# Kernel tuning notes

Hardware: AMD Instinct MI355X
Metric: run time of the kernel (lower is better)

## Reference

```python
import jax, jax.numpy as jnp
import numpy as np

D_MODEL = 1024
N_HEADS = 16
HEAD_DIM = D_MODEL // N_HEADS
WINDOW = 512


def _rope(q, k, seq_len, head_dim):
    # interleaved RoPE, identical to the torch implementation
    theta = 1.0 / 10000.0 ** (jnp.arange(0, head_dim, 2, dtype=jnp.float32) / head_dim)
    pos = jnp.arange(seq_len, dtype=jnp.float32)
    freqs = jnp.outer(pos, theta)                      # [S, hD/2]
    cos_f = jnp.cos(freqs)[None, None]                 # [1,1,S,hD/2]
    sin_f = jnp.sin(freqs)[None, None]

    def rotate(x):
        x1, x2 = x[..., ::2], x[..., 1::2]
        return jnp.stack([x1 * cos_f - x2 * sin_f, x1 * sin_f + x2 * cos_f], axis=-1).reshape(x.shape)

    return rotate(q), rotate(k)


def _sliding_window_attn(q, k, v, W, scale):
    # chunked O(S*W) causal sliding-window attention
    B, nH, S, hD = q.shape
    n_chunks = (S + W - 1) // W
    pad_s = n_chunks * W - S
    k_pad = jnp.pad(k, ((0, 0), (0, 0), (W, pad_s), (0, 0)))
    v_pad = jnp.pad(v, ((0, 0), (0, 0), (W, pad_s), (0, 0)))
    q_pad = jnp.pad(q, ((0, 0), (0, 0), (0, pad_s), (0, 0)))
    q_c = q_pad.reshape(B, nH, n_chunks, W, hD)
    k_r = k_pad.reshape(B, nH, n_chunks + 1, W, hD)
    v_r = v_pad.reshape(B, nH, n_chunks + 1, W, hD)
    # window i = chunks [i, i+1] of the left-padded sequence (== torch unfold)
    k_c = jnp.concatenate([k_r[:, :, :-1], k_r[:, :, 1:]], axis=3)  # [B,nH,C,2W,hD]
    v_c = jnp.concatenate([v_r[:, :, :-1], v_r[:, :, 1:]], axis=3)
    attn = jnp.einsum('bhcqd,bhckd->bhcqk', q_c, k_c) * scale

    qi = jnp.arange(W)[:, None]
    ki = jnp.arange(2 * W)[None, :]
    cw_mask = (ki <= qi) | (ki > qi + W)               # [W, 2W]
    chunk_idx = jnp.arange(n_chunks)[:, None]
    abs_k = chunk_idx * W + ki - W                     # [C, 2W]
    pad_mask = (abs_k < 0) | (abs_k >= S)
    q_pos = jnp.arange(n_chunks * W).reshape(n_chunks, W)
    full_mask = cw_mask[None] | pad_mask[:, None, :] | (q_pos >= S)[..., None]  # [C,W,2W]

    attn = jnp.where(full_mask[None, None], -jnp.inf, attn)
    attn = jax.nn.softmax(attn, axis=-1)
    attn = jnp.nan_to_num(attn, nan=0.0)
    out = jnp.einsum('bhcqk,bhckd->bhcqd', attn, v_c)
    return out.reshape(B, nH, n_chunks * W, hD)[:, :, :S]


def _rmsnorm(x, w):
    eps = jnp.finfo(x.dtype).eps
    return x * jax.lax.rsqrt(jnp.mean(x * x, axis=-1, keepdims=True) + eps) * w


def _sdpa(q, k, v, scale):
    s = jnp.einsum('bhqd,bhkd->bhqk', q, k) * scale
    return jnp.einsum('bhqk,bhkd->bhqd', jax.nn.softmax(s, axis=-1), v)


def setup_inputs() -> dict:
    key = jax.random.key(0)
    ks = jax.random.split(key, 11)
    D = D_MODEL
    std = 0.02
    return {
        'x': jax.random.normal(ks[0], (2, 4096, D), jnp.float32),
        'landmarks': jax.random.normal(ks[1], (2, 256, D), jnp.float32),
        'archived_landmarks': jax.random.normal(ks[2], (2, 128, D), jnp.float32),
        'W_qkv': jax.random.normal(ks[3], (D, 3 * D), jnp.float32) * std,
        'W_lm': jax.random.normal(ks[4], (D, 2 * D), jnp.float32) * std,
        'W_arch': jax.random.normal(ks[5], (D, 2 * D), jnp.float32) * std,
        'W_o': jax.random.normal(ks[6], (D, D), jnp.float32) * std,
        'W_gate': jax.random.normal(ks[7], (3 * D, 2 * D), jnp.float32) * std,
        'g_local': jnp.ones((D,), jnp.float32),
        'g_lm': jnp.ones((D,), jnp.float32),
        'g_arch': jnp.ones((D,), jnp.float32),
    }


def reference(x, landmarks, archived_landmarks, W_qkv, W_lm, W_arch, W_o, W_gate, g_local, g_lm, g_arch):
    B, S, D = x.shape
    nH, hD = N_HEADS, HEAD_DIM
    scale = hD ** -0.5

    def rsh(t, L):
        return jnp.transpose(t.reshape(B, L, nH, hD), (0, 2, 1, 3))

    q, k, v = jnp.split(x @ W_qkv, 3, axis=-1)
    Q, K, V = rsh(q, S), rsh(k, S), rsh(v, S)
    Q, K = _rope(Q, K, S, hD)

    Weff = min(WINDOW, S)
    out_loc = _sliding_window_attn(Q, K, V, Weff, scale)  # S > Weff -> chunked path
    out_loc = _rmsnorm(jnp.transpose(out_loc, (0, 2, 1, 3)).reshape(B, S, D), g_local)

    L = landmarks.shape[1]
    K_lm, V_lm = jnp.split(landmarks @ W_lm, 2, axis=-1)
    out_lm = _sdpa(Q, rsh(K_lm, L), rsh(V_lm, L), scale)
    out_lm = _rmsnorm(jnp.transpose(out_lm, (0, 2, 1, 3)).reshape(B, S, D), g_lm)

    A = archived_landmarks.shape[1]
    K_a, V_a = jnp.split(archived_landmarks @ W_arch, 2, axis=-1)
    out_a = _sdpa(Q, rsh(K_a, A), rsh(V_a, A), scale)
    out_a = _rmsnorm(jnp.transpose(out_a, (0, 2, 1, 3)).reshape(B, S, D), g_arch)

    concat = jnp.concatenate([out_loc, out_lm, out_a], axis=-1)
    gate, value = jnp.split(concat @ W_gate, 2, axis=-1)
    return (jax.nn.silu(gate) * value) @ W_o
```

## Files before the change

### kernel.cpp

```cpp
#include <hip/hip_runtime.h>
#include <cstdint>
#include <cstddef>

typedef __bf16 bf16;
typedef __bf16 bf16x2 __attribute__((ext_vector_type(2)));
typedef __bf16 bf16x4 __attribute__((ext_vector_type(4)));
typedef __bf16 bf16x8 __attribute__((ext_vector_type(8)));
typedef float  f32x2 __attribute__((ext_vector_type(2)));
typedef float  f32x4 __attribute__((ext_vector_type(4)));

#define DEVFN __device__ __forceinline__
#define BAR()  asm volatile("s_barrier" ::: "memory")
#define VMW0() asm volatile("s_waitcnt vmcnt(0)" ::: "memory")
#define VMW3() asm volatile("s_waitcnt vmcnt(3)" ::: "memory")
#define VMW4() asm volatile("s_waitcnt vmcnt(4)" ::: "memory")
#define MFMA16 __builtin_amdgcn_mfma_f32_16x16x32_bf16

DEVFN void gld_lds16(void* lds, const void* g) {
  __builtin_amdgcn_global_load_lds(
      (__attribute__((address_space(1))) void*)g,
      (__attribute__((address_space(3))) void*)lds,
      16, 0, 0);
}

__global__ void cast_f32_bf16(const float* __restrict__ in, bf16* __restrict__ out, int n4) {
  int i = blockIdx.x * blockDim.x + threadIdx.x;
  if (i < n4) {
    f32x4 v = reinterpret_cast<const f32x4*>(in)[i];
    bf16x4 o;
    o[0] = (bf16)v[0]; o[1] = (bf16)v[1]; o[2] = (bf16)v[2]; o[3] = (bf16)v[3];
    reinterpret_cast<bf16x4*>(out)[i] = o;
  }
}

__global__ void transpose_cast(const float* __restrict__ in, bf16* __restrict__ out,
                               int R, int C) {
  __shared__ float t[32][33];
  int tx = threadIdx.x, ty = threadIdx.y;
  int c = blockIdx.x * 32 + tx;
  #pragma unroll
  for (int j = 0; j < 4; ++j) {
    int r = blockIdx.y * 32 + ty + j * 8;
    t[ty + j * 8][tx] = in[(size_t)r * C + c];
  }
  __syncthreads();
  int rr = blockIdx.y * 32 + tx;
  #pragma unroll
  for (int j = 0; j < 4; ++j) {
    int cc = blockIdx.x * 32 + ty + j * 8;
    out[(size_t)cc * R + rr] = (bf16)t[tx][ty + j * 8];
  }
}

__global__ void rope_table(float* __restrict__ tab) {
  int idx = blockIdx.x * 256 + threadIdx.x;
  int s = idx >> 5, i = idx & 31;
  float theta = powf(10000.f, -(float)(2 * i) * (1.f / 64.f));
  float f = (float)s * theta;
  tab[idx * 2]     = cosf(f);
  tab[idx * 2 + 1] = sinf(f);
}

__global__ __launch_bounds__(512) void gemm_gate4(
    const bf16* __restrict__ A, const bf16* __restrict__ Bt,
    bf16* __restrict__ G, int K) {
  __shared__ alignas(16) bf16 lds[2][2][2][256 * 32];
  const int tid = threadIdx.x;
  const int w = tid >> 6, l = tid & 63;
  const int l15 = l & 15, lg = l >> 4;
  const int wm = w >> 2, wn = w & 3;
  const int nwg = gridDim.x, qx = nwg >> 3;
  const int swz = (blockIdx.x & 7) * qx + (blockIdx.x >> 3);
  const int m0 = (swz >> 3) << 8;
  const int n0 = (swz & 7) << 7;
  const int nt = K >> 6;

  auto stage = [&](int b, int ab, int kk, int t) {
    const int k0 = (t << 6) + (kk << 5);
    #pragma unroll
    for (int i = 0; i < 2; ++i) {
      int u = i * 512 + tid;
      int row = u >> 2, slot = u & 3;
      int ss = slot ^ ((row >> 1) & 3);
      int grow;
      if (ab) {
        int q = row >> 6, o = row & 63;
        grow = (o < 32) ? (n0 + q * 32 + o) : (1024 + n0 + q * 32 + o - 32);
      } else {
        grow = m0 + row;
      }
      const bf16* src = ab ? Bt : A;
      gld_lds16(&lds[b][ab][kk][(i * 512 + w * 64) * 8],
                src + (size_t)grow * K + k0 + ss * 8);
    }
  };
  auto rd = [&](int b, int ab, int kk, int r) -> bf16x8 {
    return *reinterpret_cast<const bf16x8*>(
        &lds[b][ab][kk][(r << 5) + ((lg ^ ((r >> 1) & 3)) << 3)]);
  };

  f32x4 acc[8][4] = {};
  bf16x8 aLo[4], aHi[4], bfr[4];

  stage(0, 0, 0, 0);
  stage(0, 1, 0, 0);
  stage(0, 0, 1, 0);
  stage(0, 1, 1, 0);
  VMW4();
  BAR();

  for (int t = 0; t < nt; ++t) {
    const int c = t & 1;
    const bool st = (t + 1) < nt;
    #pragma unroll
    for (int f = 0; f < 4; ++f) aLo[f] = rd(c, 0, 0, wm * 128 + f * 16 + l15);
    #pragma unroll
    for (int f = 0; f < 4; ++f) bfr[f] = rd(c, 1, 0, wn * 64 + f * 16 + l15);
    if (st) stage(c ^ 1, 0, 0, t + 1);
    BAR();
    __builtin_amdgcn_s_setprio(1);
    #pragma unroll
    for (int mi = 0; mi < 4; ++mi)
      #pragma unroll
      for (int ni = 0; ni < 4; ++ni)
        acc[mi][ni] = MFMA16(aLo[mi], bfr[ni], acc[mi][ni], 0, 0, 0);
    __builtin_amdgcn_s_setprio(0);
    #pragma unroll
    for (int f = 0; f < 4; ++f) aHi[f] = rd(c, 0, 0, wm * 128 + (f + 4) * 16 + l15);
    BAR();
    if (st) stage(c ^ 1, 1, 0, t + 1);
    BAR();
    __builtin_amdgcn_s_setprio(1);
    #pragma unroll
    for (int mi = 0; mi < 4; ++mi)
      #pragma unroll
      for (int ni = 0; ni < 4; ++ni)
        acc[mi + 4][ni] = MFMA16(aHi[mi], bfr[ni], acc[mi + 4][ni], 0, 0, 0);
    __builtin_amdgcn_s_setprio(0);
    if (st) { VMW4(); } else { VMW0(); }
    BAR();
    #pragma unroll
    for (int f = 0; f < 4; ++f) aLo[f] = rd(c, 0, 1, wm * 128 + f * 16 + l15);
    #pragma unroll
    for (int f = 0; f < 4; ++f) bfr[f] = rd(c, 1, 1, wn * 64 + f * 16 + l15);
    if (st) stage(c ^ 1, 0, 1, t + 1);
    BAR();
    __builtin_amdgcn_s_setprio(1);
    #pragma unroll
    for (int mi = 0; mi < 4; ++mi)
      #pragma unroll
      for (int ni = 0; ni < 4; ++ni)
        acc[mi][ni] = MFMA16(aLo[mi], bfr[ni], acc[mi][ni], 0, 0, 0);
    __builtin_amdgcn_s_setprio(0);
    #pragma unroll
    for (int f = 0; f < 4; ++f) aHi[f] = rd(c, 0, 1, wm * 128 + (f + 4) * 16 + l15);
    BAR();
    if (st) stage(c ^ 1, 1, 1, t + 1);
    BAR();
    __builtin_amdgcn_s_setprio(1);
    #pragma unroll
    for (int mi = 0; mi < 4; ++mi)
      #pragma unroll
      for (int ni = 0; ni < 4; ++ni)
        acc[mi + 4][ni] = MFMA16(aHi[mi], bfr[ni], acc[mi + 4][ni], 0, 0, 0);
    __builtin_amdgcn_s_setprio(0);
    VMW4();
    BAR();
  }

  #pragma unroll
  for (int mi = 0; mi < 8; ++mi) {
    #pragma unroll
    for (int r = 0; r < 4; ++r) {
      int row = m0 + wm * 128 + mi * 16 + lg * 4 + r;
      bf16* grow = G + (size_t)row * 1024 + n0 + wn * 32 + l15;
      #pragma unroll
      for (int ni = 0; ni < 2; ++ni) {
        float g = acc[mi][ni][r], v = acc[mi][ni + 2][r];
        grow[ni * 16] = (bf16)((g / (1.f + __expf(-g))) * v);
      }
    }
  }
}

template<typename OT>
__global__ __launch_bounds__(512) void gemm256n128(
    const bf16* __restrict__ A, const bf16* __restrict__ Bt, OT* __restrict__ C,
    int M, int N, int K) {
  __shared__ alignas(16) bf16 ldsA[2][2][256 * 32];
  __shared__ alignas(16) bf16 ldsB[2][2][128 * 32];
  const int tid = threadIdx.x;
  const int w = tid >> 6, l = tid & 63;
  const int l15 = l & 15, lg = l >> 4;
  const int wm = w >> 1, wn = w & 1;
  const int nwg = gridDim.x, qx = nwg >> 3;
  const int swz = (blockIdx.x & 7) * qx + (blockIdx.x >> 3);
  const int gx = N >> 7;
  const int m0 = (swz / gx) << 8;
  const int n0 = (swz % gx) << 7;
  const int nt = K >> 6;

  auto stageA = [&](int b, int kk, int t) {
    const int k0 = (t << 6) + (kk << 5);
    #pragma unroll
    for (int i = 0; i < 2; ++i) {
      int u = i * 512 + tid;
      int row = u >> 2, slot = u & 3;
      int ss = slot ^ ((row >> 1) & 3);
      gld_lds16(&ldsA[b][kk][(i * 512 + w * 64) * 8],
                A + (size_t)(m0 + row) * K + k0 + ss * 8);
    }
  };
  auto stageB = [&](int b, int kk, int t) {
    const int k0 = (t << 6) + (kk << 5);
    int row = tid >> 2, slot = tid & 3;
    int ss = slot ^ ((row >> 1) & 3);
    gld_lds16(&ldsB[b][kk][(w * 64) * 8],
              Bt + (size_t)(n0 + row) * K + k0 + ss * 8);
  };
  auto rdA = [&](int b, int kk, int r) -> bf16x8 {
    return *reinterpret_cast<const bf16x8*>(
        &ldsA[b][kk][(r << 5) + ((lg ^ ((r >> 1) & 3)) << 3)]);
  };
  auto rdB = [&](int b, int kk, int r) -> bf16x8 {
    return *reinterpret_cast<const bf16x8*>(
        &ldsB[b][kk][(r << 5) + ((lg ^ ((r >> 1) & 3)) << 3)]);
  };

  f32x4 acc[4][4] = {};
  bf16x8 af[4], bf[4];

  stageA(0, 0, 0); stageB(0, 0, 0);
  stageA(0, 1, 0); stageB(0, 1, 0);
  VMW3();
  BAR();

  for (int t = 0; t < nt; ++t) {
    const int c = t & 1;
    const bool st = (t + 1) < nt;
    #pragma unroll
    for (int kk = 0; kk < 2; ++kk) {
      #pragma unroll
      for (int f = 0; f < 4; ++f) af[f] = rdA(c, kk, wm * 64 + f * 16 + l15);
      #pragma unroll
      for (int f = 0; f < 4; ++f) bf[f] = rdB(c, kk, wn * 64 + f * 16 + l15);
      if (st) { stageA(c ^ 1, kk, t + 1); stageB(c ^ 1, kk, t + 1); }
      BAR();
      __builtin_amdgcn_s_setprio(1);
      #pragma unroll
      for (int mi = 0; mi < 4; ++mi)
        #pragma unroll
        for (int ni = 0; ni < 4; ++ni)
          acc[mi][ni] = MFMA16(af[mi], bf[ni], acc[mi][ni], 0, 0, 0);
      __builtin_amdgcn_s_setprio(0);
      if (st) { VMW3(); }
      else if (kk == 0) { VMW0(); }
      BAR();
    }
  }

  #pragma unroll
  for (int mi = 0; mi < 4; ++mi) {
    #pragma unroll
    for (int r = 0; r < 4; ++r) {
      int row = m0 + wm * 64 + mi * 16 + lg * 4 + r;
      OT* crow = C + (size_t)row * N + n0 + wn * 64 + l15;
      #pragma unroll
      for (int ni = 0; ni < 4; ++ni) crow[ni * 16] = (OT)acc[mi][ni][r];
    }
  }
}

__global__ __launch_bounds__(256) void gemm_skt(
    const bf16* __restrict__ A, const bf16* __restrict__ Bt, float* __restrict__ C,
    int M, int N, int Ktot, int Kc) {
  __shared__ alignas(16) bf16 As[128 * 64];
  __shared__ alignas(16) bf16 Bs[128 * 64];
  int tid = threadIdx.x;
  int w = tid >> 6, l = tid & 63;
  int l15 = l & 15, lg = l >> 4;
  int m0 = blockIdx.y * 128;
  int n0 = blockIdx.x * 128;
  int sk = blockIdx.z;
  int kb = sk * Kc;
  float* Cs = C + (size_t)sk * M * N;
  int wr = (w >> 1) * 64, wc = (w & 1) * 64;
  f32x4 acc[4][4] = {};
  int nk = Kc >> 6;
  for (int kt = 0; kt < nk; ++kt) {
    int k0 = kb + (kt << 6);
    #pragma unroll
    for (int it = 0; it < 4; ++it) {
      int c = it * 256 + tid;
      int row = c >> 3, c8 = c & 7;
      gld_lds16(&As[(size_t)(it * 256 + w * 64) * 8],
                A + (size_t)(m0 + row) * Ktot + k0 + c8 * 8);
      gld_lds16(&Bs[(size_t)(it * 256 + w * 64) * 8],
                Bt + (size_t)(n0 + row) * Ktot + k0 + c8 * 8);
    }
    __syncthreads();
    #pragma unroll
    for (int kk = 0; kk < 64; kk += 32) {
      bf16x8 a[4], b[4];
      #pragma unroll
      for (int i = 0; i < 4; ++i)
        a[i] = *reinterpret_cast<const bf16x8*>(&As[(wr + i * 16 + l15) * 64 + kk + lg * 8]);
      #pragma unroll
      for (int i = 0; i < 4; ++i)
        b[i] = *reinterpret_cast<const bf16x8*>(&Bs[(wc + i * 16 + l15) * 64 + kk + lg * 8]);
      #pragma unroll
      for (int mi = 0; mi < 4; ++mi)
        #pragma unroll
        for (int ni = 0; ni < 4; ++ni)
          acc[mi][ni] = MFMA16(a[mi], b[ni], acc[mi][ni], 0, 0, 0);
    }
    __syncthreads();
  }
  #pragma unroll
  for (int mi = 0; mi < 4; ++mi) {
    #pragma unroll
    for (int r = 0; r < 4; ++r) {
      int row = m0 + wr + mi * 16 + lg * 4 + r;
      float* crow = Cs + (size_t)row * N + n0 + wc + l15;
      #pragma unroll
      for (int ni = 0; ni < 4; ++ni) crow[ni * 16] = acc[mi][ni][r];
    }
  }
}

__global__ void rope_qk(const bf16* __restrict__ qkv, const float* __restrict__ tab,
                        bf16* __restrict__ Qb, bf16* __restrict__ Kb) {
  int idx = blockIdx.x * 256 + threadIdx.x;
  int i = idx & 31;
  int h = (idx >> 5) & 15;
  int bs = idx >> 9;
  int s = bs & 4095;
  int b = bs >> 12;
  const bf16* row = qkv + (size_t)bs * 3072;
  bf16x2 q2 = *reinterpret_cast<const bf16x2*>(row + h * 64 + 2 * i);
  bf16x2 k2 = *reinterpret_cast<const bf16x2*>(row + 1024 + h * 64 + 2 * i);
  f32x2 cs = *reinterpret_cast<const f32x2*>(tab + s * 64 + 2 * i);
  float c = cs[0], sn = cs[1];
  float q0 = (float)q2[0], q1 = (float)q2[1];
  float k0 = (float)k2[0], k1 = (float)k2[1];
  size_t ob = (((size_t)(b * 16 + h) * 4096) + s) * 64 + 2 * i;
  bf16x2 qo, ko;
  qo[0] = (bf16)((q0 * c - q1 * sn) * 0.125f);
  qo[1] = (bf16)((q0 * sn + q1 * c) * 0.125f);
  ko[0] = (bf16)(k0 * c - k1 * sn);
  ko[1] = (bf16)(k0 * sn + k1 * c);
  *reinterpret_cast<bf16x2*>(Qb + ob) = qo;
  *reinterpret_cast<bf16x2*>(Kb + ob) = ko;
}

__global__ void kv_post(const bf16* __restrict__ kv, bf16* __restrict__ Kdst,
                        bf16* __restrict__ Vt, int Lk, int rs, int koff, int voff) {
  __shared__ float t[64][65];
  int s0 = blockIdx.x * 64;
  int h = blockIdx.y, b = blockIdx.z;
  int tid = threadIdx.x;
  int lane_d = tid & 63;
  int rq = tid >> 6;
  const bf16* base = kv + (size_t)b * Lk * rs;
  if (Kdst) {
    #pragma unroll
    for (int r = 0; r < 16; ++r) {
      int si = r * 4 + rq;
      Kdst[(((size_t)(b * 16 + h) * Lk) + s0 + si) * 64 + lane_d] =
          base[(size_t)(s0 + si) * rs + koff + h * 64 + lane_d];
    }
  }
  #pragma unroll
  for (int r = 0; r < 16; ++r) {
    int si = r * 4 + rq;
    t[si][lane_d] = (float)base[(size_t)(s0 + si) * rs + voff + h * 64 + lane_d];
  }
  __syncthreads();
  #pragma unroll
  for (int r = 0; r < 16; ++r) {
    int d = r * 4 + rq;
    Vt[(((size_t)(b * 16 + h) * 64) + d) * Lk + s0 + lane_d] = (bf16)t[lane_d][d];
  }
}

__global__ void kv_post4(const float* __restrict__ kv, bf16* __restrict__ Kdst,
                         bf16* __restrict__ Vt, int Lk, int Mtot) {
  __shared__ float t[64][65];
  int s0 = blockIdx.x * 64;
  int h = blockIdx.y, b = blockIdx.z;
  int tid = threadIdx.x;
  int lane_d = tid & 63;
  int rq = tid >> 6;
  const size_t slab = (size_t)Mtot * 2048;
  const float* base = kv + (size_t)b * Lk * 2048;
  #pragma unroll
  for (int r = 0; r < 16; ++r) {
    int si = r * 4 + rq;
    size_t o = (size_t)(s0 + si) * 2048 + h * 64 + lane_d;
    float kvv = base[o] + base[slab + o] + base[2 * slab + o] + base[3 * slab + o];
    size_t ov = o + 1024;
    float vvv = base[ov] + base[slab + ov] + base[2 * slab + ov] + base[3 * slab + ov];
    Kdst[(((size_t)(b * 16 + h) * Lk) + s0 + si) * 64 + lane_d] = (bf16)kvv;
    t[si][lane_d] = vvv;
  }
  __syncthreads();
  #pragma unroll
  for (int r = 0; r < 16; ++r) {
    int d = r * 4 + rq;
    Vt[(((size_t)(b * 16 + h) * 64) + d) * Lk + s0 + lane_d] = (bf16)t[lane_d][d];
  }
}

__global__ __launch_bounds__(256) void attn64(
    const bf16* __restrict__ Qb, const bf16* __restrict__ Kb,
    const bf16* __restrict__ Vt, bf16* __restrict__ outc) {
  constexpr int S = 4096;
  __shared__ alignas(16) bf16 Ks[2][64 * 64];
  __shared__ alignas(16) bf16 Vs[2][64 * 64];
  __shared__ alignas(16) bf16 Ps[4][16 * 72];
  int tid = threadIdx.x;
  int w = tid >> 6, l = tid & 63;
  int l15 = l & 15, lg = l >> 4;
  int qt = blockIdx.x, h = blockIdx.y, b = blockIdx.z;

  size_t qrow = (((size_t)(b * 16 + h) * S) + qt * 64 + w * 16 + l15) * 64;
  bf16x8 qf[2];
  qf[0] = *reinterpret_cast<const bf16x8*>(Qb + qrow + lg * 8);
  qf[1] = *reinterpret_cast<const bf16x8*>(Qb + qrow + 32 + lg * 8);
  const bf16* Kbase = Kb + ((size_t)(b * 16 + h) * S) * 64;
  const bf16* Vbase = Vt + ((size_t)(b * 16 + h) * 64) * S;

  float mrow = -1e30f, lsum = 0.f;
  f32x4 acc[4] = {};

  const int kt_hi = qt;
  const int kt_lo = qt >= 8 ? qt - 8 : 0;

  auto stage = [&](int buf, int kt) {
    const bf16* kg = Kbase + (size_t)kt * 64 * 64;
    #pragma unroll
    for (int it = 0; it < 2; ++it) {
      int u = it * 256 + tid;
      int row = u >> 3, sl = u & 7;
      gld_lds16(&Ks[buf][(it * 256 + w * 64) * 8], kg + row * 64 + (sl ^ (row & 7)) * 8);
    }
    #pragma unroll
    for (int it = 0; it < 2; ++it) {
      int u = it * 256 + tid;
      int row = u >> 3, sl = u & 7;
      gld_lds16(&Vs[buf][(it * 256 + w * 64) * 8],
                Vbase + (size_t)row * S + kt * 64 + (sl ^ (row & 7)) * 8);
    }
  };

  stage(0, kt_hi);

  int i = 0;
  for (int kt = kt_hi; kt >= kt_lo; --kt, ++i) {
    const int buf = i & 1;
    if (kt > kt_lo) { stage(buf ^ 1, kt - 1); VMW4(); } else { VMW0(); }
    BAR();

    f32x4 st[4] = {};
    #pragma unroll
    for (int kk = 0; kk < 2; ++kk) {
      #pragma unroll
      for (int f = 0; f < 4; ++f) {
        bf16x8 kf = *reinterpret_cast<const bf16x8*>(
            &Ks[buf][(f * 16 + l15) * 64 + (((kk * 4 + lg) ^ (l15 & 7)) << 3)]);
        st[f] = MFMA16(kf, qf[kk], st[f], 0, 0, 0);
      }
    }

    int qi = w * 16 + l15;
    if (kt == qt) {
      #pragma unroll
      for (int f = 0; f < 4; ++f)
        #pragma unroll
        for (int r = 0; r < 4; ++r)
          if (f * 16 + lg * 4 + r > qi) st[f][r] = -1e30f;
    } else if (kt == qt - 8) {
      #pragma unroll
      for (int f = 0; f < 4; ++f)
        #pragma unroll
        for (int r = 0; r < 4; ++r)
          if (f * 16 + lg * 4 + r <= qi) st[f][r] = -1e30f;
    }

    float rm = -1e30f;
    #pragma unroll
    for (int f = 0; f < 4; ++f)
      #pragma unroll
      for (int r = 0; r < 4; ++r) rm = fmaxf(rm, st[f][r]);
    rm = fmaxf(rm, __shfl_xor(rm, 16));
    rm = fmaxf(rm, __shfl_xor(rm, 32));
    float mnew = fmaxf(mrow, rm);
    float fsc = __expf(mrow - mnew);
    float ps = 0.f;
    #pragma unroll
    for (int f = 0; f < 4; ++f) {
      bf16x4 pv;
      #pragma unroll
      for (int r = 0; r < 4; ++r) {
        float p = __expf(st[f][r] - mnew);
        ps += p;
        pv[r] = (bf16)p;
      }
      *reinterpret_cast<bf16x4*>(&Ps[w][l15 * 72 + f * 16 + lg * 4]) = pv;
    }
    ps += __shfl_xor(ps, 16);
    ps += __shfl_xor(ps, 32);
    lsum = lsum * fsc + ps;
    mrow = mnew;

    #pragma unroll
    for (int r = 0; r < 4; ++r) {
      float fr = __shfl(fsc, lg * 4 + r);
      #pragma unroll
      for (int f = 0; f < 4; ++f) acc[f][r] *= fr;
    }

    #pragma unroll
    for (int kk = 0; kk < 2; ++kk) {
      bf16x8 pa = *reinterpret_cast<const bf16x8*>(&Ps[w][l15 * 72 + kk * 32 + lg * 8]);
      #pragma unroll
      for (int f = 0; f < 4; ++f) {
        bf16x8 vf = *reinterpret_cast<const bf16x8*>(
            &Vs[buf][(f * 16 + l15) * 64 + (((kk * 4 + lg) ^ (l15 & 7)) << 3)]);
        acc[f] = MFMA16(pa, vf, acc[f], 0, 0, 0);
      }
    }
    BAR();
  }

  float inv = 1.f / lsum;
  #pragma unroll
  for (int r = 0; r < 4; ++r) {
    float ir = __shfl(inv, lg * 4 + r);
    int srow = qt * 64 + w * 16 + lg * 4 + r;
    bf16* orow = outc + ((size_t)b * S + srow) * 3072 + h * 64 + l15;
    #pragma unroll
    for (int f = 0; f < 4; ++f) orow[f * 16] = (bf16)(acc[f][r] * ir);
  }
}

template<int LKV, int NQI>
__global__ __launch_bounds__(512) void attn_res(
    const bf16* __restrict__ Qb, const bf16* __restrict__ Kb,
    const bf16* __restrict__ Vt, bf16* __restrict__ outc, int col_off) {
  constexpr int S = 4096;
  __shared__ alignas(16) bf16 Ks[LKV * 64];
  __shared__ alignas(16) bf16 Vs[64 * LKV];
  __shared__ alignas(16) bf16 Ps[8][2][16 * 72];
  const int tid = threadIdx.x;
  const int w = tid >> 6, l = tid & 63;
  const int l15 = l & 15, lg = l >> 4;
  const int h = blockIdx.y, b = blockIdx.z;
  const bf16* Kg = Kb + ((size_t)(b * 16 + h) * LKV) * 64;
  const bf16* Vg = Vt + ((size_t)(b * 16 + h) * 64) * LKV;

  constexpr int NU = LKV / 64;
  constexpr int SPR = LKV / 8;
  #pragma unroll
  for (int i = 0; i < NU; ++i) {
    int u = i * 512 + tid;
    int row = u >> 3, sl = u & 7;
    gld_lds16(&Ks[(i * 512 + w * 64) * 8], Kg + row * 64 + (sl ^ (row & 7)) * 8);
  }
  #pragma unroll
  for (int i = 0; i < NU; ++i) {
    int u = i * 512 + tid;
    int row = u / SPR, sl = u % SPR;
    gld_lds16(&Vs[(i * 512 + w * 64) * 8],
              Vg + (size_t)row * LKV + ((sl & ~7) + ((sl & 7) ^ (row & 7))) * 8);
  }
  __syncthreads();

  for (int qi = 0; qi < NQI; ++qi) {
    const int Q0 = (blockIdx.x * NQI + qi) * 256 + w * 32;
    bf16x8 qf[2][2];
    #pragma unroll
    for (int c = 0; c < 2; ++c) {
      size_t qrow = (((size_t)(b * 16 + h) * S) + Q0 + c * 16 + l15) * 64;
      qf[c][0] = *reinterpret_cast<const bf16x8*>(Qb + qrow + lg * 8);
      qf[c][1] = *reinterpret_cast<const bf16x8*>(Qb + qrow + 32 + lg * 8);
    }
    float mrow[2] = {-30000.f, -30000.f}, lsum[2] = {0.f, 0.f};
    f32x4 acc[2][4] = {};

    #pragma unroll
    for (int kt = 0; kt < LKV / 64; ++kt) {
      f32x4 st[2][4] = {};
      #pragma unroll
      for (int kk = 0; kk < 2; ++kk) {
        #pragma unroll
        for (int f = 0; f < 4; ++f) {
          bf16x8 kf = *reinterpret_cast<const bf16x8*>(
              &Ks[(kt * 64 + f * 16 + l15) * 64 + (((kk * 4 + lg) ^ (l15 & 7)) << 3)]);
          #pragma unroll
          for (int c = 0; c < 2; ++c)
            st[c][f] = MFMA16(kf, qf[c][kk], st[c][f], 0, 0, 0);
        }
      }
      #pragma unroll
      for (int c = 0; c < 2; ++c) {
        float rm = -1e30f;
        #pragma unroll
        for (int f = 0; f < 4; ++f)
          #pragma unroll
          for (int r = 0; r < 4; ++r) rm = fmaxf(rm, st[c][f][r]);
        rm = fmaxf(rm, __shfl_xor(rm, 16));
        rm = fmaxf(rm, __shfl_xor(rm, 32));
        float mnew = fmaxf(mrow[c], rm);
        float fsc = __expf(mrow[c] - mnew);
        float ps = 0.f;
        #pragma unroll
        for (int f = 0; f < 4; ++f) {
          bf16x4 pv;
          #pragma unroll
          for (int r = 0; r < 4; ++r) {
            float p = __expf(st[c][f][r] - mnew);
            ps += p;
            pv[r] = (bf16)p;
          }
          *reinterpret_cast<bf16x4*>(&Ps[w][c][l15 * 72 + f * 16 + lg * 4]) = pv;
        }
        ps += __shfl_xor(ps, 16);
        ps += __shfl_xor(ps, 32);
        lsum[c] = lsum[c] * fsc + ps;
        mrow[c] = mnew;
        #pragma unroll
        for (int r = 0; r < 4; ++r) {
          float fr = __shfl(fsc, lg * 4 + r);
          #pragma unroll
          for (int f = 0; f < 4; ++f) acc[c][f][r] *= fr;
        }
      }
      #pragma unroll
      for (int kk = 0; kk < 2; ++kk) {
        bf16x8 pa[2];
        #pragma unroll
        for (int c = 0; c < 2; ++c)
          pa[c] = *reinterpret_cast<const bf16x8*>(&Ps[w][c][l15 * 72 + kk * 32 + lg * 8]);
        #pragma unroll
        for (int f = 0; f < 4; ++f) {
          bf16x8 vf = *reinterpret_cast<const bf16x8*>(
              &Vs[(f * 16 + l15) * LKV + ((kt * 8 + ((kk * 4 + lg) ^ (l15 & 7))) << 3)]);
          #pragma unroll
          for (int c = 0; c < 2; ++c)
            acc[c][f] = MFMA16(pa[c], vf, acc[c][f], 0, 0, 0);
        }
      }
    }

    #pragma unroll
    for (int c = 0; c < 2; ++c) {
      float inv = 1.f / lsum[c];
      #pragma unroll
      for (int r = 0; r < 4; ++r) {
        float ir = __shfl(inv, lg * 4 + r);
        int srow = Q0 + c * 16 + lg * 4 + r;
        bf16* orow = outc + ((size_t)b * S + srow) * 3072 + col_off + h * 64 + l15;
        #pragma unroll
        for (int f = 0; f < 4; ++f) orow[f * 16] = (bf16)(acc[c][f][r] * ir);
      }
    }
  }
}

__global__ __launch_bounds__(256) void rmsnorm_kernel(
    bf16* data, const float* __restrict__ g0,
    const float* __restrict__ g1, const float* __restrict__ g2) {
  int token = blockIdx.x;
  int seg = blockIdx.y;
  const float* g = seg == 0 ? g0 : (seg == 1 ? g1 : g2);
  int tid = threadIdx.x;
  size_t base = (size_t)token * 3072 + seg * 1024;
  bf16x4 bv = reinterpret_cast<const bf16x4*>(data + base)[tid];
  f32x4 v;
  #pragma unroll
  for (int j = 0; j < 4; ++j) v[j] = (float)bv[j];
  float ss = v[0] * v[0] + v[1] * v[1] + v[2] * v[2] + v[3] * v[3];
  #pragma unroll
  for (int m = 1; m < 64; m <<= 1) ss += __shfl_xor(ss, m);
  __shared__ float red[4];
  if ((tid & 63) == 0) red[tid >> 6] = ss;
  __syncthreads();
  float tot = red[0] + red[1] + red[2] + red[3];
  float sc = rsqrtf(tot * (1.f / 1024.f) + 1.19209290e-07f);
  f32x4 gv = reinterpret_cast<const f32x4*>(g)[tid];
  bf16x4 o;
  #pragma unroll
  for (int j = 0; j < 4; ++j) o[j] = (bf16)(v[j] * sc * gv[j]);
  reinterpret_cast<bf16x4*>(data + base)[tid] = o;
}

extern "C" void kernel_launch(void* const* d_in, const int* in_sizes, int n_in,
                              void* d_out, int out_size, void* d_ws, size_t ws_size,
                              hipStream_t stream) {
  (void)in_sizes; (void)n_in; (void)out_size; (void)ws_size;
  const float* x       = (const float*)d_in[0];
  const float* lm      = (const float*)d_in[1];
  const float* arch    = (const float*)d_in[2];
  const float* W_qkv   = (const float*)d_in[3];
  const float* W_lm    = (const float*)d_in[4];
  const float* W_arch  = (const float*)d_in[5];
  const float* W_o     = (const float*)d_in[6];
  const float* W_gate  = (const float*)d_in[7];
  const float* g_local = (const float*)d_in[8];
  const float* g_lm    = (const float*)d_in[9];
  const float* g_arch  = (const float*)d_in[10];
  float* out = (float*)d_out;

  char* ws = (char*)d_ws;
  size_t off = 0;
  auto alloc = [&](size_t bytes) -> void* {
    void* p = ws + off;
    off += (bytes + 255) & ~(size_t)255;
    return p;
  };
  bf16*  Wqkv_t   = (bf16*) alloc(3072ull * 1024 * 2);
  bf16*  Wlm_t    = (bf16*) alloc(2048ull * 1024 * 2);
  bf16*  Warch_t  = (bf16*) alloc(2048ull * 1024 * 2);
  bf16*  Wgate_t  = (bf16*) alloc(2048ull * 3072 * 2);
  bf16*  Wo_t     = (bf16*) alloc(1024ull * 1024 * 2);
  bf16*  lm_bf    = (bf16*) alloc(512ull * 1024 * 2);
  bf16*  arch_bf  = (bf16*) alloc(256ull * 1024 * 2);
  float* ropetab  = (float*)alloc(4096ull * 64 * 4);
  bf16*  Klm      = (bf16*) alloc(2ull * 16 * 256 * 64 * 2);
  bf16*  Vlm_t    = (bf16*) alloc(2ull * 16 * 64 * 256 * 2);
  bf16*  Ka       = (bf16*) alloc(2ull * 16 * 128 * 64 * 2);
  bf16*  Va_t     = (bf16*) alloc(2ull * 16 * 64 * 128 * 2);
  char* R1 = (char*)alloc(24ull * 1024 * 1024);
  bf16*  x_bf   = (bf16*)R1;
  float* lmP    = (float*)R1;
  float* archP  = (float*)(R1 + 16ull * 1024 * 1024);
  bf16*  gated  = (bf16*)R1;
  char* R2 = (char*)alloc(8192ull * 3072 * 2);
  bf16* qkv_bf  = (bf16*)R2;
  bf16* concatb = (bf16*)R2;
  char* R3 = (char*)alloc(3ull * 16 * 1024 * 1024);
  bf16* Qb = (bf16*)R3;
  bf16* Kb = (bf16*)(R3 + 16ull * 1024 * 1024);
  bf16* Vt = (bf16*)(R3 + 32ull * 1024 * 1024);

  transpose_cast<<<dim3(96, 32), dim3(32, 8), 0, stream>>>(W_qkv, Wqkv_t, 1024, 3072);
  transpose_cast<<<dim3(64, 32), dim3(32, 8), 0, stream>>>(W_lm, Wlm_t, 1024, 2048);
  transpose_cast<<<dim3(64, 32), dim3(32, 8), 0, stream>>>(W_arch, Warch_t, 1024, 2048);
  transpose_cast<<<dim3(64, 96), dim3(32, 8), 0, stream>>>(W_gate, Wgate_t, 3072, 2048);
  transpose_cast<<<dim3(32, 32), dim3(32, 8), 0, stream>>>(W_o, Wo_t, 1024, 1024);
  cast_f32_bf16<<<8192, 256, 0, stream>>>(x, x_bf, 8192 * 1024 / 4);
  cast_f32_bf16<<<512, 256, 0, stream>>>(lm, lm_bf, 512 * 1024 / 4);
  cast_f32_bf16<<<256, 256, 0, stream>>>(arch, arch_bf, 256 * 1024 / 4);
  rope_table<<<512, 256, 0, stream>>>(ropetab);

  gemm256n128<bf16><<<768, 512, 0, stream>>>(x_bf, Wqkv_t, qkv_bf, 8192, 3072, 1024);
  gemm_skt<<<dim3(16, 4, 4), 256, 0, stream>>>(lm_bf, Wlm_t, lmP, 512, 2048, 1024, 256);
  gemm_skt<<<dim3(16, 2, 4), 256, 0, stream>>>(arch_bf, Warch_t, archP, 256, 2048, 1024, 256);

  rope_qk<<<16384, 256, 0, stream>>>(qkv_bf, ropetab, Qb, Kb);
  kv_post<<<dim3(64, 16, 2), 256, 0, stream>>>(qkv_bf, nullptr, Vt, 4096, 3072, 0, 2048);
  kv_post4<<<dim3(4, 16, 2), 256, 0, stream>>>(lmP, Klm, Vlm_t, 256, 512);
  kv_post4<<<dim3(2, 16, 2), 256, 0, stream>>>(archP, Ka, Va_t, 128, 256);

  attn64<<<dim3(64, 16, 2), 256, 0, stream>>>(Qb, Kb, Vt, concatb);
  attn_res<256, 2><<<dim3(8, 16, 2), 512, 0, stream>>>(Qb, Klm, Vlm_t, concatb, 1024);
  attn_res<128, 2><<<dim3(8, 16, 2), 512, 0, stream>>>(Qb, Ka, Va_t, concatb, 2048);

  rmsnorm_kernel<<<dim3(8192, 3), 256, 0, stream>>>(concatb, g_local, g_lm, g_arch);

  gemm_gate4<<<256, 512, 0, stream>>>(concatb, Wgate_t, gated, 3072);
  gemm256n128<float><<<256, 512, 0, stream>>>(gated, Wo_t, out, 8192, 1024, 1024);
}
```

Baseline: 456.2 us.

## Restructure GEMM pipeline to four-stage ring buffer with three-deep prefetch

```diff
diff --git a/kernel.cpp b/kernel.cpp
--- a/kernel.cpp
+++ b/kernel.cpp
@@ -14,6 +14,7 @@
 #define VMW0() asm volatile("s_waitcnt vmcnt(0)" ::: "memory")
 #define VMW3() asm volatile("s_waitcnt vmcnt(3)" ::: "memory")
 #define VMW4() asm volatile("s_waitcnt vmcnt(4)" ::: "memory")
+#define VMW6() asm volatile("s_waitcnt vmcnt(6)" ::: "memory")
 #define MFMA16 __builtin_amdgcn_mfma_f32_16x16x32_bf16
 
 DEVFN void gld_lds16(void* lds, const void* g) {
@@ -184,11 +185,11 @@
 }
 
 template<typename OT>
-__global__ __launch_bounds__(512) void gemm256n128(
+__global__ __launch_bounds__(512) void gemmK128(
     const bf16* __restrict__ A, const bf16* __restrict__ Bt, OT* __restrict__ C,
-    int M, int N, int K) {
-  __shared__ alignas(16) bf16 ldsA[2][2][256 * 32];
-  __shared__ alignas(16) bf16 ldsB[2][2][128 * 32];
+    int N, int K) {
+  __shared__ alignas(16) bf16 ldsA[4][256 * 32];
+  __shared__ alignas(16) bf16 ldsB[4][128 * 32];
   const int tid = threadIdx.x;
   const int w = tid >> 6, l = tid & 63;
   const int l15 = l & 15, lg = l >> 4;
@@ -198,65 +199,63 @@
   const int gx = N >> 7;
   const int m0 = (swz / gx) << 8;
   const int n0 = (swz % gx) << 7;
-  const int nt = K >> 6;
-
-  auto stageA = [&](int b, int kk, int t) {
-    const int k0 = (t << 6) + (kk << 5);
+  const int ns = K >> 5;
+
+  auto stage = [&](int s) {
+    const int buf = s & 3;
+    const int k0 = s << 5;
     #pragma unroll
     for (int i = 0; i < 2; ++i) {
       int u = i * 512 + tid;
       int row = u >> 2, slot = u & 3;
       int ss = slot ^ ((row >> 1) & 3);
-      gld_lds16(&ldsA[b][kk][(i * 512 + w * 64) * 8],
+      gld_lds16(&ldsA[buf][(i * 512 + w * 64) * 8],
                 A + (size_t)(m0 + row) * K + k0 + ss * 8);
     }
+    {
+      int row = tid >> 2, slot = tid & 3;
+      int ss = slot ^ ((row >> 1) & 3);
+      gld_lds16(&ldsB[buf][(w * 64) * 8],
+                Bt + (size_t)(n0 + row) * K + k0 + ss * 8);
+    }
   };
-  auto stageB = [&](int b, int kk, int t) {
-    const int k0 = (t << 6) + (kk << 5);
-    int row = tid >> 2, slot = tid & 3;
-    int ss = slot ^ ((row >> 1) & 3);
-    gld_lds16(&ldsB[b][kk][(w * 64) * 8],
-              Bt + (size_t)(n0 + row) * K + k0 + ss * 8);
+  auto rdA = [&](int buf, int r) -> bf16x8 {
+    return *reinterpret_cast<const bf16x8*>(
+        &ldsA[buf][(r << 5) + ((lg ^ ((r >> 1) & 3)) << 3)]);
   };
-  auto rdA = [&](int b, int kk, int r) -> bf16x8 {
+  auto rdB = [&](int buf, int r) -> bf16x8 {
     return *reinterpret_cast<const bf16x8*>(
-        &ldsA[b][kk][(r << 5) + ((lg ^ ((r >> 1) & 3)) << 3)]);
+        &ldsB[buf][(r << 5) + ((lg ^ ((r >> 1) & 3)) << 3)]);
   };
-  auto rdB = [&](int b, int kk, int r) -> bf16x8 {
-    return *reinterpret_cast<const bf16x8*>(
-        &ldsB[b][kk][(r << 5) + ((lg ^ ((r >> 1) & 3)) << 3)]);
-  };
 
   f32x4 acc[4][4] = {};
-  bf16x8 af[4], bf[4];
-
-  stageA(0, 0, 0); stageB(0, 0, 0);
-  stageA(0, 1, 0); stageB(0, 1, 0);
-  VMW3();
+
+  stage(0); stage(1); stage(2);
+  VMW6();
   BAR();
 
-  for (int t = 0; t < nt; ++t) {
-    const int c = t & 1;
-    const bool st = (t + 1) < nt;
-    #pragma unroll
-    for (int kk = 0; kk < 2; ++kk) {
-      #pragma unroll
-      for (int f = 0; f < 4; ++f) af[f] = rdA(c, kk, wm * 64 + f * 16 + l15);
-      #pragma unroll
-      for (int f = 0; f < 4; ++f) bf[f] = rdB(c, kk, wn * 64 + f * 16 + l15);
-      if (st) { stageA(c ^ 1, kk, t + 1); stageB(c ^ 1, kk, t + 1); }
-      BAR();
-      __builtin_amdgcn_s_setprio(1);
-      #pragma unroll
-      for (int mi = 0; mi < 4; ++mi)
-        #pragma unroll
-        for (int ni = 0; ni < 4; ++ni)
-          acc[mi][ni] = MFMA16(af[mi], bf[ni], acc[mi][ni], 0, 0, 0);
-      __builtin_amdgcn_s_setprio(0);
-      if (st) { VMW3(); }
-      else if (kk == 0) { VMW0(); }
-      BAR();
-    }
+  for (int s = 0; s < ns; ++s) {
+    const int c = s & 3;
+    bf16x8 af[4], bf[4];
+    #pragma unroll
+    for (int f = 0; f < 4; ++f) af[f] = rdA(c, wm * 64 + f * 16 + l15);
+    #pragma unroll
+    for (int f = 0; f < 4; ++f) bf[f] = rdB(c, wn * 64 + f * 16 + l15);
+    const bool st3 = (s + 3) < ns;
+    if (st3) stage(s + 3);
+    BAR();
+    __builtin_amdgcn_s_setprio(1);
+    #pragma unroll
+    for (int mi = 0; mi < 4; ++mi)
+      #pragma unroll
+      for (int ni = 0; ni < 4; ++ni)
+        acc[mi][ni] = MFMA16(af[mi], bf[ni], acc[mi][ni], 0, 0, 0);
+    __builtin_amdgcn_s_setprio(0);
+    const int rem = ns - 1 - s;
+    if (st3) { VMW6(); }
+    else if (rem == 2) { VMW3(); }
+    else if (rem == 1) { VMW0(); }
+    BAR();
   }
 
   #pragma unroll
@@ -754,7 +753,7 @@
   cast_f32_bf16<<<256, 256, 0, stream>>>(arch, arch_bf, 256 * 1024 / 4);
   rope_table<<<512, 256, 0, stream>>>(ropetab);
 
-  gemm256n128<bf16><<<768, 512, 0, stream>>>(x_bf, Wqkv_t, qkv_bf, 8192, 3072, 1024);
+  gemmK128<bf16><<<768, 512, 0, stream>>>(x_bf, Wqkv_t, qkv_bf, 3072, 1024);
   gemm_skt<<<dim3(16, 4, 4), 256, 0, stream>>>(lm_bf, Wlm_t, lmP, 512, 2048, 1024, 256);
   gemm_skt<<<dim3(16, 2, 4), 256, 0, stream>>>(arch_bf, Warch_t, archP, 256, 2048, 1024, 256);
 
@@ -770,5 +769,5 @@
   rmsnorm_kernel<<<dim3(8192, 3), 256, 0, stream>>>(concatb, g_local, g_lm, g_arch);
 
   gemm_gate4<<<256, 512, 0, stream>>>(concatb, Wgate_t, gated, 3072);
-  gemm256n128<float><<<256, 512, 0, stream>>>(gated, Wo_t, out, 8192, 1024, 1024);
-}
+  gemmK128<float><<<256, 512, 0, stream>>>(gated, Wo_t, out, 1024, 1024);
+}
```

Result: no change. 456.1 us (-0.0%).
